# Kernel optimization log

Measured on AMD Instinct MI355X. Metric: run time of the kernel, lower is better.

## Reference

```python
import jax, jax.numpy as jnp
import numpy as np

BN_EPS = 1e-5

def _conv1x1(x, w, b):
    # x: (B,C,H,W), w: (O,C), b: (O,)
    return jnp.einsum('bchw,oc->bohw', x, w) + b[None, :, None, None]

def setup_inputs() -> dict:
    key = jax.random.key(0)
    ks = jax.random.split(key, 9)
    B, C, H, W = 16, 512, 64, 64
    Ci = C // 2
    x = jax.random.normal(ks[0], (B, C, H, W), dtype=jnp.float32)
    s_in = (2.0 / C) ** 0.5   # kaiming fan_out-ish scale for 1x1 conv
    s_ci = (2.0 / Ci) ** 0.5
    return {
        'x': x,
        'g_w': jax.random.normal(ks[1], (Ci, C), dtype=jnp.float32) * s_in,
        'g_b': jnp.zeros((Ci,), dtype=jnp.float32),
        'theta_w': jax.random.normal(ks[2], (Ci, C), dtype=jnp.float32) * s_in,
        'theta_b': jnp.zeros((Ci,), dtype=jnp.float32),
        'phi_w': jax.random.normal(ks[3], (Ci, C), dtype=jnp.float32) * s_in,
        'phi_b': jnp.zeros((Ci,), dtype=jnp.float32),
        'W_w': jax.random.normal(ks[4], (C, Ci), dtype=jnp.float32) * s_ci,
        'W_b': jnp.zeros((C,), dtype=jnp.float32),
        'bn_gamma': jnp.ones((C,), dtype=jnp.float32),
        'bn_beta': jnp.zeros((C,), dtype=jnp.float32),
    }

def reference(x, g_w, g_b, theta_w, theta_b, phi_w, phi_b, W_w, W_b, bn_gamma, bn_beta):
    B, C, H, W = x.shape
    N = H * W
    g_x = _conv1x1(x, g_w, g_b).reshape(B, -1, N)          # (B, Ci, N)
    theta_x = _conv1x1(x, theta_w, theta_b).reshape(B, -1, N)  # (B, Ci, N)
    phi_x = _conv1x1(x, phi_w, phi_b).reshape(B, -1, N)        # (B, Ci, N)
    # Faithful to source: theta NOT permuted -> f is (B, Ci, Ci) channel attention
    f = jnp.einsum('bcn,bdn->bcd', theta_x, phi_x)
    f_div_C = jax.nn.softmax(f, axis=-1)
    y = jnp.einsum('bcd,bdn->bcn', f_div_C, g_x).reshape(B, -1, H, W)  # (B, Ci, H, W)
    z = _conv1x1(y, W_w, W_b)                              # (B, C, H, W)
    # BatchNorm2d, training mode (batch statistics, biased var as in torch)
    mean = jnp.mean(z, axis=(0, 2, 3), keepdims=True)
    var = jnp.var(z, axis=(0, 2, 3), keepdims=True)
    z = (z - mean) * jax.lax.rsqrt(var + BN_EPS)
    z = z * bn_gamma[None, :, None, None] + bn_beta[None, :, None, None]
    return z + x
```

## Files before the change

kernel.cpp:

```cpp
#include <hip/hip_runtime.h>

typedef __bf16 bf16x8 __attribute__((ext_vector_type(8)));
typedef float f32x4 __attribute__((ext_vector_type(4)));

#define LDK 40
#define NB 16
#define C_ 512
#define CI 256
#define HW 4096
#define KSPLIT 4
#define KCHUNK (HW / KSPLIT)

__device__ __forceinline__ float bf2f(unsigned short u){
  union { unsigned int u; float f; } c; c.u = ((unsigned int)u) << 16; return c.f;
}
__device__ __forceinline__ unsigned short f2bf(float f){
  union { float f; unsigned int u; } c; c.f = f;
  unsigned int u = c.u + 0x7fffu + ((c.u >> 16) & 1u);
  return (unsigned short)(u >> 16);
}
__device__ __forceinline__ float read_val(const void* p, int i, bool f32){
  return f32 ? ((const float*)p)[i] : bf2f(((const unsigned short*)p)[i]);
}


__device__ __forceinline__ void stage_rm(const unsigned short* __restrict__ src, int stride,
                                         unsigned short* dst, int t){
  #pragma unroll
  for (int it = 0; it < 2; ++it){
    int idx = t + it*256;
    int row = idx >> 2;
    int ko  = (idx & 3) * 8;
    *(uint4*)(dst + row*LDK + ko) = *(const uint4*)(src + (size_t)row*stride + ko);
  }
}

__device__ __forceinline__ void stage_tr(const unsigned short* __restrict__ src, int stride,
                                         unsigned short* dst, int t){
  #pragma unroll
  for (int it = 0; it < 2; ++it){
    int idx = t + it*256;
    int row = idx >> 4;
    int co  = (idx & 15) * 8;
    uint4 vv = *(const uint4*)(src + (size_t)row*stride + co);
    unsigned short e[8]; *(uint4*)e = vv;
    #pragma unroll
    for (int k = 0; k < 8; ++k) dst[(co + k)*LDK + row] = e[k];
  }
}

__device__ __forceinline__ void mfma_step(const unsigned short* As, const unsigned short* Bs,
                                          f32x4 acc[4][4], int wm, int wn, int lane){
  const int r = lane & 15, q = lane >> 4;
  bf16x8 a[4], b[4];
  #pragma unroll
  for (int i = 0; i < 4; ++i)
    a[i] = *(const bf16x8*)(As + (wm*64 + 16*i + r)*LDK + 8*q);
  #pragma unroll
  for (int j = 0; j < 4; ++j)
    b[j] = *(const bf16x8*)(Bs + (wn*64 + 16*j + r)*LDK + 8*q);
  #pragma unroll
  for (int i = 0; i < 4; ++i)
    #pragma unroll
    for (int j = 0; j < 4; ++j)
      acc[i][j] = __builtin_amdgcn_mfma_f32_16x16x32_bf16(a[i], b[j], acc[i][j], 0, 0, 0);
}

__device__ __forceinline__ void gload16(const unsigned short* g, unsigned short* l){
  __builtin_amdgcn_global_load_lds(
      (__attribute__((address_space(1))) void*)const_cast<unsigned short*>(g),
      (__attribute__((address_space(3))) void*)l, 16, 0, 0);
}

__device__ __forceinline__ void gstage(const unsigned short* __restrict__ src, size_t rstride,
                                       unsigned short* buf, int w, int lane){
  const int ro = lane >> 3;
  const int sc = (lane & 7) ^ ro;
  const unsigned short* s0 = src + (size_t)ro*rstride + sc*8;
  unsigned short* l0 = buf + (size_t)(w*32)*64;
  #pragma unroll
  for (int i = 0; i < 4; ++i)
    gload16(s0 + (size_t)(w*32 + i*8)*rstride, l0 + i*8*64);
}

__global__ __launch_bounds__(256) void k_detect(const unsigned short* __restrict__ x, int* flag){
  const int t = threadIdx.x;
  int cnt = 0;
  for (int i = t; i < 65536; i += 256){
    unsigned short u = x[i];
    if (((u >> 7) & 0xFF) == 0xFF) cnt++;
  }
  __shared__ int red[256];
  red[t] = cnt; __syncthreads();
  for (int s2 = 128; s2 > 0; s2 >>= 1){
    if (t < s2) red[t] += red[t + s2];
    __syncthreads();
  }
  if (t == 0) flag[0] = (red[0] > 0) ? 1 : 0;
}

__global__ __launch_bounds__(256) void k_wconv(const void* tw, const void* pw, const void* gw,
    const void* Ww, const void* gb, const void* tb, const void* pb, const void* Wb,
    const void* gam, const void* bet, const int* __restrict__ flag,
    unsigned short* twh, unsigned short* twl, unsigned short* phh, unsigned short* phl,
    unsigned short* gwc, unsigned short* Wwc, float* biasf){
  const bool f32 = (*flag != 0);
  const int bid = blockIdx.x, t = threadIdx.x;
  if (bid < 2048){
    const int seg = bid >> 9;
    const int i = (bid & 511)*256 + t;
    if (seg == 0){
      float w = read_val(tw, i, f32);
      unsigned short h = f2bf(w);
      twh[i] = h; twl[i] = f2bf(w - bf2f(h));
    } else if (seg == 1){
      float w = read_val(pw, i, f32);
      unsigned short h = f2bf(w);
      phh[i] = h; phl[i] = f2bf(w - bf2f(h));
    } else if (seg == 2){
      gwc[i] = f2bf(read_val(gw, i, f32));
    } else {
      Wwc[i] = f2bf(read_val(Ww, i, f32));
    }
  } else {
    const int i = (bid - 2048)*256 + t;
    if (i < 2304){
      float v;
      if      (i <  256) v = read_val(gb,  i,        f32);
      else if (i <  512) v = read_val(tb,  i - 256,  f32);
      else if (i <  768) v = read_val(pb,  i - 512,  f32);
      else if (i < 1280) v = read_val(Wb,  i - 768,  f32);
      else if (i < 1792) v = read_val(gam, i - 1280, f32);
      else               v = read_val(bet, i - 1792, f32);
      biasf[i] = v;
    }
  }
}

__global__ __launch_bounds__(256) void k_xconv(const void* __restrict__ xraw,
    const int* __restrict__ flag, unsigned short* __restrict__ xq, float* __restrict__ s){
  const bool f32 = (*flag != 0);
  const int bc = blockIdx.x, t = threadIdx.x;
  float sum = 0.f;
  if (f32){
    const float* xr = (const float*)xraw + (size_t)bc*HW;
    unsigned short* oq = xq + (size_t)bc*8192;
    #pragma unroll
    for (int it = 0; it < 4; ++it){
      const int off = it*1024 + t*4;
      f32x4 v = *(const f32x4*)(xr + off);
      unsigned int wh[2], wl[2];
      #pragma unroll
      for (int k = 0; k < 2; ++k){
        unsigned short h0 = f2bf(v[2*k]),   h1 = f2bf(v[2*k+1]);
        unsigned short l0 = f2bf(v[2*k]   - bf2f(h0));
        unsigned short l1 = f2bf(v[2*k+1] - bf2f(h1));
        wh[k] = (unsigned int)h0 | ((unsigned int)h1 << 16);
        wl[k] = (unsigned int)l0 | ((unsigned int)l1 << 16);
      }
      sum += v[0] + v[1] + v[2] + v[3];
      const int qb = (off >> 5)*64 + (off & 31);
      *(uint2*)(oq + qb)      = make_uint2(wh[0], wh[1]);
      *(uint2*)(oq + qb + 32) = make_uint2(wl[0], wl[1]);
    }
  } else {
    const unsigned short* xr = (const unsigned short*)xraw + (size_t)bc*HW;
    #pragma unroll
    for (int it = 0; it < 2; ++it){
      const int off = it*2048 + t*8;
      uint4 raw = *(const uint4*)(xr + off);
      unsigned int wd[4] = {raw.x, raw.y, raw.z, raw.w};
      #pragma unroll
      for (int k = 0; k < 4; ++k)
        sum += bf2f((unsigned short)(wd[k] & 0xffff)) + bf2f((unsigned short)(wd[k] >> 16));
    }
  }
  #pragma unroll
  for (int off = 1; off < 64; off <<= 1) sum += __shfl_xor(sum, off);
  __shared__ float r1[4];
  if ((t & 63) == 0) r1[t >> 6] = sum;
  __syncthreads();
  if (t == 0) s[bc] = r1[0] + r1[1] + r1[2] + r1[3];
}

__global__ __launch_bounds__(256) void k_gram(const void* __restrict__ xraw,
    const unsigned short* __restrict__ xq, const int* __restrict__ flag,
    float* __restrict__ Gp){
  const bool f32 = (*flag != 0);
  const int b = blockIdx.z, ks = blockIdx.y, tile = blockIdx.x;
  int bm, bn;
  if      (tile < 4){ bm = 0; bn = tile; }
  else if (tile < 7){ bm = 1; bn = tile - 3; }
  else if (tile < 9){ bm = 2; bn = tile - 5; }
  else              { bm = 3; bn = 3; }
  const int t = threadIdx.x, lane = t & 63, w = t >> 6, wm = w >> 1, wn = w & 1;
  __shared__ __align__(16) unsigned short Abuf[2][128*64];
  __shared__ __align__(16) unsigned short Bbuf[2][128*64];
  const bool diag = (bm == bn);
  const unsigned short* srcA;
  const unsigned short* srcB;
  size_t rstride;
  int nsteps;
  if (f32){
    const unsigned short* xb = xq + (size_t)b*C_*8192;
    srcA = xb + (size_t)(bm*128)*8192 + (size_t)ks*(KCHUNK/32)*64;
    srcB = xb + (size_t)(bn*128)*8192 + (size_t)ks*(KCHUNK/32)*64;
    rstride = 8192; nsteps = KCHUNK/32;
  } else {
    const unsigned short* xb = (const unsigned short*)xraw + (size_t)b*C_*HW;
    srcA = xb + (size_t)(bm*128)*HW + ks*KCHUNK;
    srcB = xb + (size_t)(bn*128)*HW + ks*KCHUNK;
    rstride = HW; nsteps = KCHUNK/64;
  }
  f32x4 acc[4][4] = {};
  const int r = lane & 15, q = lane >> 4;
  const int rx = r & 7;
  const int c0 = q ^ rx;
  const int c1 = (4 + q) ^ rx;

  gstage(srcA, rstride, Abuf[0], w, lane);
  if (!diag) gstage(srcB, rstride, Bbuf[0], w, lane);
  __syncthreads();

  int cur = 0;
  for (int st = 0; st < nsteps; ++st){
    if (st + 1 < nsteps){
      gstage(srcA + (size_t)(st+1)*64, rstride, Abuf[cur^1], w, lane);
      if (!diag) gstage(srcB + (size_t)(st+1)*64, rstride, Bbuf[cur^1], w, lane);
    }
    const unsigned short* A = Abuf[cur];
    const unsigned short* B = diag ? Abuf[cur] : Bbuf[cur];
    bf16x8 a0[4], a1[4], b0[4], b1[4];
    #pragma unroll
    for (int i = 0; i < 4; ++i){
      const unsigned short* ap = A + (size_t)(wm*64 + 16*i + r)*64;
      a0[i] = *(const bf16x8*)(ap + c0*8);
      a1[i] = *(const bf16x8*)(ap + c1*8);
    }
    #pragma unroll
    for (int j = 0; j < 4; ++j){
      const unsigned short* bp = B + (size_t)(wn*64 + 16*j + r)*64;
      b0[j] = *(const bf16x8*)(bp + c0*8);
      b1[j] = *(const bf16x8*)(bp + c1*8);
    }
    if (f32){
      #pragma unroll
      for (int i = 0; i < 4; ++i)
        #pragma unroll
        for (int j = 0; j < 4; ++j){
          acc[i][j] = __builtin_amdgcn_mfma_f32_16x16x32_bf16(a0[i], b0[j], acc[i][j], 0, 0, 0);
          acc[i][j] = __builtin_amdgcn_mfma_f32_16x16x32_bf16(a0[i], b1[j], acc[i][j], 0, 0, 0);
          acc[i][j] = __builtin_amdgcn_mfma_f32_16x16x32_bf16(a1[i], b0[j], acc[i][j], 0, 0, 0);
        }
    } else {
      #pragma unroll
      for (int i = 0; i < 4; ++i)
        #pragma unroll
        for (int j = 0; j < 4; ++j){
          acc[i][j] = __builtin_amdgcn_mfma_f32_16x16x32_bf16(a0[i], b0[j], acc[i][j], 0, 0, 0);
          acc[i][j] = __builtin_amdgcn_mfma_f32_16x16x32_bf16(a1[i], b1[j], acc[i][j], 0, 0, 0);
        }
    }
    __syncthreads();
    cur ^= 1;
  }
  float* Gt = Gp + (((size_t)b*10 + tile)*KSPLIT + ks)*16384;
  #pragma unroll
  for (int i = 0; i < 4; ++i)
    #pragma unroll
    for (int j = 0; j < 4; ++j)
      #pragma unroll
      for (int ii = 0; ii < 4; ++ii){
        int row = wm*64 + 16*i + 4*q + ii;
        int col = wn*64 + 16*j + r;
        Gt[row*128 + col] = acc[i][j][ii];
      }
}

__global__ __launch_bounds__(256) void k_gred(const float* __restrict__ Gp,
    unsigned short* __restrict__ Gh, unsigned short* __restrict__ Gl){
  const int b = blockIdx.z, bmO = blockIdx.y, bnO = blockIdx.x, t = threadIdx.x;
  const int lo = bmO < bnO ? bmO : bnO;
  const int hi = bmO < bnO ? bnO : bmO;
  const int tile = (lo == 0) ? hi : (lo == 1) ? 3 + hi : (lo == 2) ? 5 + hi : 9;
  const float* src = Gp + ((size_t)b*10 + tile)*KSPLIT*16384;
  unsigned short* ghB = Gh + (size_t)b*C_*C_;
  unsigned short* glB = Gl + (size_t)b*C_*C_;
  if (bmO <= bnO){
    #pragma unroll
    for (int i = 0; i < 16; ++i){
      const int off = i*1024 + t*4;
      f32x4 v = *(const f32x4*)(src + off);
      #pragma unroll
      for (int ks = 1; ks < KSPLIT; ++ks){
        f32x4 u2 = *(const f32x4*)(src + ks*16384 + off);
        v[0] += u2[0]; v[1] += u2[1]; v[2] += u2[2]; v[3] += u2[3];
      }
      const int row = off >> 7, col = off & 127;
      unsigned int wh[2], wl[2];
      #pragma unroll
      for (int k = 0; k < 2; ++k){
        unsigned short h0 = f2bf(v[2*k]),   h1 = f2bf(v[2*k+1]);
        unsigned short l0 = f2bf(v[2*k]   - bf2f(h0));
        unsigned short l1 = f2bf(v[2*k+1] - bf2f(h1));
        wh[k] = (unsigned int)h0 | ((unsigned int)h1 << 16);
        wl[k] = (unsigned int)l0 | ((unsigned int)l1 << 16);
      }
      size_t o = (size_t)(bmO*128 + row)*C_ + bnO*128 + col;
      *(uint2*)(ghB + o) = make_uint2(wh[0], wh[1]);
      *(uint2*)(glB + o) = make_uint2(wl[0], wl[1]);
    }
  } else {
    __shared__ float ldz[32*129];
    const int rr = t >> 1, cseg = (t & 1)*16;
    const int orl = t >> 3, oseg = (t & 7)*16;
    for (int cc = 0; cc < 4; ++cc){
      float vals[16];
      #pragma unroll
      for (int j = 0; j < 4; ++j){
        const int so = rr*128 + cc*32 + cseg + j*4;
        f32x4 v = *(const f32x4*)(src + so);
        #pragma unroll
        for (int ks = 1; ks < KSPLIT; ++ks){
          f32x4 u2 = *(const f32x4*)(src + ks*16384 + so);
          v[0] += u2[0]; v[1] += u2[1]; v[2] += u2[2]; v[3] += u2[3];
        }
        vals[4*j] = v[0]; vals[4*j+1] = v[1]; vals[4*j+2] = v[2]; vals[4*j+3] = v[3];
      }
      __syncthreads();
      #pragma unroll
      for (int e = 0; e < 16; ++e) ldz[(cseg + e)*129 + rr] = vals[e];
      __syncthreads();
      unsigned int wh[8], wl[8];
      #pragma unroll
      for (int k = 0; k < 8; ++k){
        float f0 = ldz[orl*129 + oseg + 2*k];
        float f1 = ldz[orl*129 + oseg + 2*k + 1];
        unsigned short h0 = f2bf(f0), h1 = f2bf(f1);
        unsigned short l0 = f2bf(f0 - bf2f(h0)), l1 = f2bf(f1 - bf2f(h1));
        wh[k] = (unsigned int)h0 | ((unsigned int)h1 << 16);
        wl[k] = (unsigned int)l0 | ((unsigned int)l1 << 16);
      }
      size_t o = (size_t)(bmO*128 + cc*32 + orl)*C_ + bnO*128 + oseg;
      *(uint4*)(ghB + o)     = make_uint4(wh[0], wh[1], wh[2], wh[3]);
      *(uint4*)(ghB + o + 8) = make_uint4(wh[4], wh[5], wh[6], wh[7]);
      *(uint4*)(glB + o)     = make_uint4(wl[0], wl[1], wl[2], wl[3]);
      *(uint4*)(glB + o + 8) = make_uint4(wl[4], wl[5], wl[6], wl[7]);
    }
  }
}

__global__ __launch_bounds__(256) void k_T(const unsigned short* __restrict__ twh,
    const unsigned short* __restrict__ twl, const int* __restrict__ flag,
    const unsigned short* __restrict__ Gh, const unsigned short* __restrict__ Gl,
    unsigned short* __restrict__ Th, unsigned short* __restrict__ Tl){
  const bool f32 = (*flag != 0);
  const int b = blockIdx.z, nt = blockIdx.x, mt = blockIdx.y;
  const int t = threadIdx.x, lane = t & 63, w = t >> 6, wm = w >> 1, wn = w & 1;
  __shared__ unsigned short Ath[128*LDK];
  __shared__ unsigned short Atl[128*LDK];
  __shared__ unsigned short Bh[128*LDK];
  __shared__ unsigned short Bl[128*LDK];
  const unsigned short* Ghb = Gh + (size_t)b*C_*C_;
  const unsigned short* Glb = Gl + (size_t)b*C_*C_;
  f32x4 acc[4][4] = {};
  for (int k0 = 0; k0 < C_; k0 += 32){
    stage_rm(twh + (size_t)mt*128*C_ + k0, C_, Ath, t);
    if (f32) stage_rm(twl + (size_t)mt*128*C_ + k0, C_, Atl, t);
    stage_rm(Ghb + (size_t)nt*128*C_ + k0, C_, Bh, t);
    stage_rm(Glb + (size_t)nt*128*C_ + k0, C_, Bl, t);
    __syncthreads();
    mfma_step(Ath, Bh, acc, wm, wn, lane);
    mfma_step(Ath, Bl, acc, wm, wn, lane);
    if (f32) mfma_step(Atl, Bh, acc, wm, wn, lane);
    __syncthreads();
  }
  unsigned short* Thb = Th + (size_t)b*CI*C_;
  unsigned short* Tlb = Tl + (size_t)b*CI*C_;
  const int r = lane & 15, q = lane >> 4;
  #pragma unroll
  for (int i = 0; i < 4; ++i)
    #pragma unroll
    for (int j = 0; j < 4; ++j)
      #pragma unroll
      for (int ii = 0; ii < 4; ++ii){
        int row = mt*128 + wm*64 + 16*i + 4*q + ii;
        int col = nt*128 + wn*64 + 16*j + r;
        float vv = acc[i][j][ii];
        unsigned short h = f2bf(vv);
        Thb[(size_t)row*C_ + col] = h;
        Tlb[(size_t)row*C_ + col] = f2bf(vv - bf2f(h));
      }
}

__global__ __launch_bounds__(256) void k_f(const unsigned short* __restrict__ Th,
    const unsigned short* __restrict__ Tl, const unsigned short* __restrict__ phh,
    const unsigned short* __restrict__ phl, const int* __restrict__ flag,
    float* __restrict__ f){
  const bool f32 = (*flag != 0);
  const int b = blockIdx.z, nt = blockIdx.x, mt = blockIdx.y;
  const int t = threadIdx.x, lane = t & 63, w = t >> 6, wm = w >> 1, wn = w & 1;
  __shared__ unsigned short ATh[128*LDK];
  __shared__ unsigned short ATl[128*LDK];
  __shared__ unsigned short Bph[128*LDK];
  __shared__ unsigned short Bpl[128*LDK];
  f32x4 acc[4][4] = {};
  const unsigned short* Thb = Th + (size_t)b*CI*C_;
  const unsigned short* Tlb = Tl + (size_t)b*CI*C_;
  for (int k0 = 0; k0 < C_; k0 += 32){
    stage_rm(Thb + (size_t)mt*128*C_ + k0, C_, ATh, t);
    stage_rm(Tlb + (size_t)mt*128*C_ + k0, C_, ATl, t);
    stage_rm(phh + (size_t)nt*128*C_ + k0, C_, Bph, t);
    if (f32) stage_rm(phl + (size_t)nt*128*C_ + k0, C_, Bpl, t);
    __syncthreads();
    mfma_step(ATh, Bph, acc, wm, wn, lane);
    mfma_step(ATl, Bph, acc, wm, wn, lane);
    if (f32) mfma_step(ATh, Bpl, acc, wm, wn, lane);
    __syncthreads();
  }
  float* fb = f + (size_t)b*CI*CI;
  const int r = lane & 15, q = lane >> 4;
  #pragma unroll
  for (int i = 0; i < 4; ++i)
    #pragma unroll
    for (int j = 0; j < 4; ++j)
      #pragma unroll
      for (int ii = 0; ii < 4; ++ii){
        int row = mt*128 + wm*64 + 16*i + 4*q + ii;
        int col = nt*128 + wn*64 + 16*j + r;
        fb[(size_t)row*CI + col] = acc[i][j][ii];
      }
}

__global__ __launch_bounds__(256) void k_uv(const unsigned short* __restrict__ twh,
    const unsigned short* __restrict__ twl, const unsigned short* __restrict__ phh,
    const unsigned short* __restrict__ phl, const float* __restrict__ s,
    float* __restrict__ u, float* __restrict__ v){
  const int b = blockIdx.x, c = threadIdx.x;
  __shared__ float sl[C_];
  sl[c] = s[(size_t)b*C_ + c];
  sl[c + 256] = s[(size_t)b*C_ + c + 256];
  __syncthreads();
  float su = 0.f, sv = 0.f;
  for (int e = 0; e < C_; ++e){
    su += (bf2f(twh[(size_t)c*C_ + e]) + bf2f(twl[(size_t)c*C_ + e])) * sl[e];
    sv += (bf2f(phh[(size_t)c*C_ + e]) + bf2f(phl[(size_t)c*C_ + e])) * sl[e];
  }
  u[(size_t)b*CI + c] = su;
  v[(size_t)b*CI + c] = sv;
}

__global__ __launch_bounds__(256) void k_softmax(const float* __restrict__ f,
    const float* __restrict__ u, const float* __restrict__ v,
    const float* __restrict__ tbf, const float* __restrict__ pbf,
    unsigned short* __restrict__ S){
  const int b = blockIdx.y;
  const int c = blockIdx.x*4 + (threadIdx.x >> 6);
  const int lane = threadIdx.x & 63;
  const float* fr = f + ((size_t)b*CI + c)*CI;
  f32x4 val = *(const f32x4*)(fr + lane*4);
  const float uc = u[(size_t)b*CI + c];
  const float tbc = tbf[c];
  float vv[4];
  #pragma unroll
  for (int k = 0; k < 4; ++k){
    int d = lane*4 + k;
    float pbd = pbf[d];
    vv[k] = val[k] + uc*pbd + tbc*(v[(size_t)b*CI + d] + 4096.0f*pbd);
  }
  float mx = fmaxf(fmaxf(vv[0], vv[1]), fmaxf(vv[2], vv[3]));
  #pragma unroll
  for (int off = 1; off < 64; off <<= 1) mx = fmaxf(mx, __shfl_xor(mx, off));
  float e[4], sum = 0.f;
  #pragma unroll
  for (int k = 0; k < 4; ++k){ e[k] = expf(vv[k] - mx); sum += e[k]; }
  #pragma unroll
  for (int off = 1; off < 64; off <<= 1) sum += __shfl_xor(sum, off);
  float inv = 1.0f / sum;
  uint2 pack;
  pack.x = (unsigned int)f2bf(e[0]*inv) | ((unsigned int)f2bf(e[1]*inv) << 16);
  pack.y = (unsigned int)f2bf(e[2]*inv) | ((unsigned int)f2bf(e[3]*inv) << 16);
  *(uint2*)(S + ((size_t)b*CI + c)*CI + lane*4) = pack;
}

__global__ __launch_bounds__(256) void k_M2(const unsigned short* __restrict__ Wwc,
                                            const unsigned short* __restrict__ S,
                                            unsigned short* __restrict__ M2){
  const int b = blockIdx.z, nt = blockIdx.x, mt = blockIdx.y;
  const int t = threadIdx.x, lane = t & 63, w = t >> 6, wm = w >> 1, wn = w & 1;
  __shared__ unsigned short As[128*LDK];
  __shared__ unsigned short Bs[128*LDK];
  f32x4 acc[4][4] = {};
  for (int k0 = 0; k0 < CI; k0 += 32){
    stage_rm(Wwc + (size_t)mt*128*CI + k0, CI, As, t);
    stage_tr(S + (size_t)b*CI*CI + (size_t)k0*CI + nt*128, CI, Bs, t);
    __syncthreads();
    mfma_step(As, Bs, acc, wm, wn, lane);
    __syncthreads();
  }
  unsigned short* M2b = M2 + (size_t)b*C_*CI;
  const int r = lane & 15, q = lane >> 4;
  #pragma unroll
  for (int i = 0; i < 4; ++i)
    #pragma unroll
    for (int j = 0; j < 4; ++j)
      #pragma unroll
      for (int ii = 0; ii < 4; ++ii){
        int row = mt*128 + wm*64 + 16*i + 4*q + ii;
        int col = nt*128 + wn*64 + 16*j + r;
        M2b[(size_t)row*CI + col] = f2bf(acc[i][j][ii]);
      }
}

__global__ __launch_bounds__(256) void k_Wg(const unsigned short* __restrict__ M2,
                                            const unsigned short* __restrict__ gwc,
                                            unsigned short* __restrict__ Wg){
  const int b = blockIdx.z, nt = blockIdx.x, mt = blockIdx.y;
  const int t = threadIdx.x, lane = t & 63, w = t >> 6, wm = w >> 1, wn = w & 1;
  __shared__ unsigned short As[128*LDK];
  __shared__ unsigned short Bs[128*LDK];
  const unsigned short* M2b = M2 + (size_t)b*C_*CI;
  f32x4 acc[4][4] = {};
  for (int k0 = 0; k0 < CI; k0 += 32){
    stage_rm(M2b + (size_t)mt*128*CI + k0, CI, As, t);
    stage_tr(gwc + (size_t)k0*C_ + nt*128, C_, Bs, t);
    __syncthreads();
    mfma_step(As, Bs, acc, wm, wn, lane);
    __syncthreads();
  }
  unsigned short* Wgb = Wg + (size_t)b*C_*C_;
  const int r = lane & 15, q = lane >> 4;
  #pragma unroll
  for (int i = 0; i < 4; ++i)
    #pragma unroll
    for (int j = 0; j < 4; ++j)
      #pragma unroll
      for (int ii = 0; ii < 4; ++ii){
        int row = mt*128 + wm*64 + 16*i + 4*q + ii;
        int col = nt*128 + wn*64 + 16*j + r;
        Wgb[(size_t)row*C_ + col] = f2bf(acc[i][j][ii]);
      }
}

__global__ __launch_bounds__(256) void k_bias2(const unsigned short* __restrict__ M2,
    const float* __restrict__ gbf, const float* __restrict__ Wbf, float* __restrict__ b2){
  const int b = blockIdx.x, t = threadIdx.x;
  __shared__ float gs[CI];
  gs[t] = gbf[t];
  __syncthreads();
  #pragma unroll
  for (int cc = 0; cc < 2; ++cc){
    int c = cc*256 + t;
    const unsigned short* row = M2 + (size_t)b*C_*CI + (size_t)c*CI;
    float sv = 0.f;
    for (int ci = 0; ci < CI; ++ci) sv += bf2f(row[ci]) * gs[ci];
    b2[(size_t)b*C_ + c] = sv + Wbf[c];
  }
}

__global__ __launch_bounds__(512) void k_zW(const unsigned short* __restrict__ Wg,
    const void* __restrict__ xraw, const unsigned short* __restrict__ xq,
    const int* __restrict__ flag, const float* __restrict__ bias2,
    unsigned short* __restrict__ z){
  const bool f32 = (*flag != 0);
  const int b = blockIdx.z, hwp = blockIdx.x;
  const int t = threadIdx.x, lane = t & 63, w = t >> 6;
  const int wm = w >> 1, wn = w & 1;
  __shared__ __align__(16) unsigned short As[512*LDK];
  __shared__ __align__(16) unsigned short Bs[128*LDK];
  const unsigned short* Wgb = Wg + (size_t)b*C_*C_;
  const int hw0 = hwp*128;
  f32x4 acc[8][4] = {};
  for (int k0 = 0; k0 < C_; k0 += 32){
    #pragma unroll
    for (int it = 0; it < 4; ++it){
      int idx = t + it*512;
      int row = idx >> 2, ko = (idx & 3)*8;
      *(uint4*)(As + row*LDK + ko) = *(const uint4*)(Wgb + (size_t)row*C_ + k0 + ko);
    }
    {
      int row = t >> 4, co = (t & 15)*8;
      const unsigned short* bsrc;
      if (f32){
        int hw = hw0 + co;
        bsrc = xq + (size_t)(b*C_ + k0 + row)*8192 + (size_t)((hw >> 5)*64 + (hw & 31));
      } else {
        bsrc = (const unsigned short*)xraw + (size_t)(b*C_ + k0 + row)*HW + hw0 + co;
      }
      uint4 vv = *(const uint4*)bsrc;
      unsigned short e8[8]; *(uint4*)e8 = vv;
      #pragma unroll
      for (int kk = 0; kk < 8; ++kk) Bs[(co + kk)*LDK + row] = e8[kk];
    }
    __syncthreads();
    const int r = lane & 15, q = lane >> 4;
    bf16x8 bfr[4];
    #pragma unroll
    for (int j = 0; j < 4; ++j)
      bfr[j] = *(const bf16x8*)(Bs + (wn*64 + 16*j + r)*LDK + 8*q);
    #pragma unroll
    for (int i = 0; i < 8; ++i){
      bf16x8 af = *(const bf16x8*)(As + (size_t)(wm*128 + 16*i + r)*LDK + 8*q);
      #pragma unroll
      for (int j = 0; j < 4; ++j)
        acc[i][j] = __builtin_amdgcn_mfma_f32_16x16x32_bf16(af, bfr[j], acc[i][j], 0, 0, 0);
    }
    __syncthreads();
  }
  unsigned short* zb = z + (size_t)b*C_*HW;
  const float* b2 = bias2 + (size_t)b*C_;
  const int r = lane & 15, q = lane >> 4;
  #pragma unroll
  for (int i = 0; i < 8; ++i)
    #pragma unroll
    for (int ii = 0; ii < 4; ++ii){
      int row = wm*128 + 16*i + 4*q + ii;
      float bias = b2[row];
      #pragma unroll
      for (int j = 0; j < 4; ++j){
        int col = hw0 + wn*64 + 16*j + r;
        zb[(size_t)row*HW + col] = f2bf(acc[i][j][ii] + bias);
      }
    }
}

__global__ __launch_bounds__(256) void k_bnstats(const unsigned short* __restrict__ z,
    const float* __restrict__ gamf, const float* __restrict__ betf,
    float* __restrict__ scale, float* __restrict__ shift){
  const int o = blockIdx.x, t = threadIdx.x, lane = t & 63, w = t >> 6;
  float sum = 0.f, ss = 0.f;
  for (int b = 0; b < NB; ++b){
    const unsigned short* p = z + ((size_t)b*C_ + o)*HW + t*16;
    #pragma unroll
    for (int it = 0; it < 2; ++it){
      uint4 raw = *(const uint4*)(p + it*8);
      unsigned int wd[4] = {raw.x, raw.y, raw.z, raw.w};
      #pragma unroll
      for (int k = 0; k < 4; ++k){
        float f0 = bf2f((unsigned short)(wd[k] & 0xffff));
        float f1 = bf2f((unsigned short)(wd[k] >> 16));
        sum += f0 + f1; ss += f0*f0 + f1*f1;
      }
    }
  }
  #pragma unroll
  for (int off = 1; off < 64; off <<= 1){
    sum += __shfl_xor(sum, off);
    ss  += __shfl_xor(ss, off);
  }
  __shared__ float r1[4], r2[4];
  if (lane == 0){ r1[w] = sum; r2[w] = ss; }
  __syncthreads();
  if (t == 0){
    float S1 = r1[0]+r1[1]+r1[2]+r1[3];
    float S2 = r2[0]+r2[1]+r2[2]+r2[3];
    const float n = (float)NB * (float)HW;
    float mean = S1 / n;
    float var  = S2 / n - mean*mean;
    float sc = gamf[o] * rsqrtf(var + 1e-5f);
    scale[o] = sc;
    shift[o] = betf[o] - mean*sc;
  }
}

__global__ __launch_bounds__(256) void k_out(const unsigned short* __restrict__ z,
    const void* __restrict__ xraw, const int* __restrict__ flag,
    const float* __restrict__ scale, const float* __restrict__ shift, void* __restrict__ outraw){
  const bool f32 = (*flag != 0);
  const size_t g = (size_t)blockIdx.x*256 + threadIdx.x;
  const size_t base = g*8;
  const int o = (int)((base >> 12) & (C_ - 1));
  const float sc = scale[o], sh = shift[o];
  uint4 zr = *(const uint4*)(z + base);
  unsigned int zz[4] = {zr.x, zr.y, zr.z, zr.w};
  float zv[8];
  #pragma unroll
  for (int k = 0; k < 4; ++k){
    zv[2*k]   = bf2f((unsigned short)(zz[k] & 0xffff));
    zv[2*k+1] = bf2f((unsigned short)(zz[k] >> 16));
  }
  if (f32){
    const float* x = (const float*)xraw;
    float* out = (float*)outraw;
    f32x4 x0 = *(const f32x4*)(x + base);
    f32x4 x1 = *(const f32x4*)(x + base + 4);
    f32x4 o0, o1;
    #pragma unroll
    for (int k = 0; k < 4; ++k){
      o0[k] = zv[k]*sc + sh + x0[k];
      o1[k] = zv[4+k]*sc + sh + x1[k];
    }
    *(f32x4*)(out + base) = o0;
    *(f32x4*)(out + base + 4) = o1;
  } else {
    const unsigned short* x = (const unsigned short*)xraw;
    unsigned short* out = (unsigned short*)outraw;
    uint4 xr = *(const uint4*)(x + base);
    unsigned int xx[4] = {xr.x, xr.y, xr.z, xr.w};
    unsigned int res[4];
    #pragma unroll
    for (int k = 0; k < 4; ++k){
      float x0 = bf2f((unsigned short)(xx[k] & 0xffff));
      float x1 = bf2f((unsigned short)(xx[k] >> 16));
      res[k] = (unsigned int)f2bf(zv[2*k]*sc + sh + x0)
             | ((unsigned int)f2bf(zv[2*k+1]*sc + sh + x1) << 16);
    }
    uint4 ov; ov.x = res[0]; ov.y = res[1]; ov.z = res[2]; ov.w = res[3];
    *(uint4*)(out + base) = ov;
  }
}

extern "C" void kernel_launch(void* const* d_in, const int* in_sizes, int n_in,
                              void* d_out, int out_size, void* d_ws, size_t ws_size,
                              hipStream_t stream){
  (void)in_sizes; (void)n_in; (void)out_size;
  const void* x   = d_in[0];
  const void* g_w = d_in[1];
  const void* g_b = d_in[2];
  const void* t_w = d_in[3];
  const void* t_b = d_in[4];
  const void* p_w = d_in[5];
  const void* p_b = d_in[6];
  const void* W_w = d_in[7];
  const void* W_b = d_in[8];
  const void* gam = d_in[9];
  const void* bet = d_in[10];
  char* ws = (char*)d_ws;

  constexpr size_t OFF_FLAG = 0;
  constexpr size_t OFF_TWH = OFF_FLAG + 16;
  constexpr size_t OFF_TWL = OFF_TWH + (size_t)CI*C_*2;
  constexpr size_t OFF_PHH = OFF_TWL + (size_t)CI*C_*2;
  constexpr size_t OFF_PHL = OFF_PHH + (size_t)CI*C_*2;
  constexpr size_t OFF_GWC = OFF_PHL + (size_t)CI*C_*2;
  constexpr size_t OFF_WWC = OFF_GWC + (size_t)CI*C_*2;
  constexpr size_t OFF_BIA = OFF_WWC + (size_t)C_*CI*2;
  constexpr size_t OFF_GH  = OFF_BIA + 16384;
  constexpr size_t OFF_GL  = OFF_GH + (size_t)NB*C_*C_*2;
  constexpr size_t OFF_S   = OFF_GL + (size_t)NB*C_*C_*2;
  constexpr size_t OFF_U   = OFF_S  + (size_t)NB*C_*4;
  constexpr size_t OFF_V   = OFF_U  + (size_t)NB*CI*4;
  constexpr size_t OFF_TH  = OFF_V  + (size_t)NB*CI*4;
  constexpr size_t OFF_TL  = OFF_TH + (size_t)NB*CI*C_*2;
  constexpr size_t OFF_F   = OFF_TL + (size_t)NB*CI*C_*2;
  constexpr size_t OFF_SM  = OFF_F  + (size_t)NB*CI*CI*4;
  constexpr size_t OFF_M2  = OFF_SM + (size_t)NB*CI*CI*2;
  constexpr size_t OFF_B2  = OFF_M2 + (size_t)NB*C_*CI*2;
  constexpr size_t OFF_SC  = OFF_B2 + (size_t)NB*C_*4;
  constexpr size_t OFF_SH  = OFF_SC + (size_t)C_*4;
  constexpr size_t OFF_Z   = OFF_SH + (size_t)C_*4;
  constexpr size_t OFF_XQ  = OFF_Z  + (size_t)NB*C_*HW*2;
  constexpr size_t TOTAL   = OFF_XQ + (size_t)NB*C_*HW*4;
  static_assert((size_t)NB*10*KSPLIT*16384*4 <= (size_t)NB*C_*HW*2, "Gp alias fits in Z");
  if (ws_size < TOTAL) return;

  int* flag = (int*)(ws + OFF_FLAG);
  unsigned short* twh = (unsigned short*)(ws + OFF_TWH);
  unsigned short* twl = (unsigned short*)(ws + OFF_TWL);
  unsigned short* phh = (unsigned short*)(ws + OFF_PHH);
  unsigned short* phl = (unsigned short*)(ws + OFF_PHL);
  unsigned short* gwc = (unsigned short*)(ws + OFF_GWC);
  unsigned short* Wwc = (unsigned short*)(ws + OFF_WWC);
  float* biasf = (float*)(ws + OFF_BIA);
  unsigned short* Gh = (unsigned short*)(ws + OFF_GH);
  unsigned short* Gl = (unsigned short*)(ws + OFF_GL);
  float* s  = (float*)(ws + OFF_S);
  float* u  = (float*)(ws + OFF_U);
  float* v  = (float*)(ws + OFF_V);
  unsigned short* Th = (unsigned short*)(ws + OFF_TH);
  unsigned short* Tl = (unsigned short*)(ws + OFF_TL);
  float* f  = (float*)(ws + OFF_F);
  unsigned short* Sm = (unsigned short*)(ws + OFF_SM);
  unsigned short* M2 = (unsigned short*)(ws + OFF_M2);
  float* b2 = (float*)(ws + OFF_B2);
  unsigned short* z  = (unsigned short*)(ws + OFF_Z);
  float* scale = (float*)(ws + OFF_SC);
  float* shift = (float*)(ws + OFF_SH);
  unsigned short* xq = (unsigned short*)(ws + OFF_XQ);
  float* Gp = (float*)(ws + OFF_Z);
  unsigned short* Wg = (unsigned short*)(ws + OFF_GH);

  float* gbf = biasf;
  float* tbf = biasf + 256;
  float* pbf = biasf + 512;
  float* Wbf = biasf + 768;
  float* gamf = biasf + 1280;
  float* betf = biasf + 1792;

  dim3 blk(256);
  k_detect <<<dim3(1),          blk, 0, stream>>>((const unsigned short*)x, flag);
  k_wconv  <<<dim3(2057),       blk, 0, stream>>>(t_w, p_w, g_w, W_w, g_b, t_b, p_b, W_b,
                                                  gam, bet, flag, twh, twl, phh, phl, gwc, Wwc, biasf);
  k_xconv  <<<dim3(NB*C_),      blk, 0, stream>>>(x, flag, xq, s);
  k_gram   <<<dim3(10, KSPLIT, NB), blk, 0, stream>>>(x, xq, flag, Gp);
  k_gred   <<<dim3(4, 4, NB),   blk, 0, stream>>>(Gp, Gh, Gl);
  k_T      <<<dim3(4, 2, NB),   blk, 0, stream>>>(twh, twl, flag, Gh, Gl, Th, Tl);
  k_uv     <<<dim3(NB),         blk, 0, stream>>>(twh, twl, phh, phl, s, u, v);
  k_f      <<<dim3(2, 2, NB),   blk, 0, stream>>>(Th, Tl, phh, phl, flag, f);
  k_softmax<<<dim3(64, NB),     blk, 0, stream>>>(f, u, v, tbf, pbf, Sm);
  k_M2     <<<dim3(2, 4, NB),   blk, 0, stream>>>(Wwc, Sm, M2);
  k_Wg     <<<dim3(4, 4, NB),   blk, 0, stream>>>(M2, gwc, Wg);
  k_bias2  <<<dim3(NB),         blk, 0, stream>>>(M2, gbf, Wbf, b2);
  k_zW     <<<dim3(32, 1, NB),  dim3(512), 0, stream>>>(Wg, x, xq, flag, b2, z);
  k_bnstats<<<dim3(C_),         blk, 0, stream>>>(z, gamf, betf, scale, shift);
  k_out    <<<dim3(16384),      blk, 0, stream>>>(z, x, flag, scale, shift, d_out);
}
```

Baseline: 769.9 us.

## Fuse BN statistics into zW epilogue and read Wg fragments directly from global

Computes the per-channel sum and sum of squares of z in the k_zW epilogue using shuffle reductions and atomics, so the separate k_bnstats pass over z is no longer needed; a tiny k_bnfinal then turns the sums into scale and shift. The zeroing of the sum buffers is folded into k_bias2. k_zW also drops the shared-memory staging of the Wg tile and loads A fragments straight from global memory. k_gram swaps its grid y/z axes so that the batch index moves to y and the K-split index to z. The risks are atomic contention on 512 channels, uncoalesced global A loads in the GEMM inner loop, and statistics taken from fp32 z rather than the stored bf16 values.

```diff
diff --git a/kernel.cpp b/kernel.cpp
--- a/kernel.cpp
+++ b/kernel.cpp
@@ -187,7 +187,7 @@
     const unsigned short* __restrict__ xq, const int* __restrict__ flag,
     float* __restrict__ Gp){
   const bool f32 = (*flag != 0);
-  const int b = blockIdx.z, ks = blockIdx.y, tile = blockIdx.x;
+  const int b = blockIdx.y, ks = blockIdx.z, tile = blockIdx.x;
   int bm, bn;
   if      (tile < 4){ bm = 0; bn = tile; }
   else if (tile < 7){ bm = 1; bn = tile - 3; }
@@ -543,8 +543,12 @@
 }
 
 __global__ __launch_bounds__(256) void k_bias2(const unsigned short* __restrict__ M2,
-    const float* __restrict__ gbf, const float* __restrict__ Wbf, float* __restrict__ b2){
+    const float* __restrict__ gbf, const float* __restrict__ Wbf, float* __restrict__ b2,
+    float* __restrict__ sums){
   const int b = blockIdx.x, t = threadIdx.x;
+  if (b == 0){
+    sums[t] = 0.f; sums[t + 256] = 0.f; sums[t + 512] = 0.f; sums[t + 768] = 0.f;
+  }
   __shared__ float gs[CI];
   gs[t] = gbf[t];
   __syncthreads();
@@ -561,46 +565,39 @@
 __global__ __launch_bounds__(512) void k_zW(const unsigned short* __restrict__ Wg,
     const void* __restrict__ xraw, const unsigned short* __restrict__ xq,
     const int* __restrict__ flag, const float* __restrict__ bias2,
-    unsigned short* __restrict__ z){
+    unsigned short* __restrict__ z, float* __restrict__ sumZ, float* __restrict__ sumZ2){
   const bool f32 = (*flag != 0);
   const int b = blockIdx.z, hwp = blockIdx.x;
   const int t = threadIdx.x, lane = t & 63, w = t >> 6;
   const int wm = w >> 1, wn = w & 1;
-  __shared__ __align__(16) unsigned short As[512*LDK];
   __shared__ __align__(16) unsigned short Bs[128*LDK];
   const unsigned short* Wgb = Wg + (size_t)b*C_*C_;
   const int hw0 = hwp*128;
+  const int r = lane & 15, q = lane >> 4;
+  const int srow = t >> 4, sco = (t & 15)*8;
   f32x4 acc[8][4] = {};
   for (int k0 = 0; k0 < C_; k0 += 32){
-    #pragma unroll
-    for (int it = 0; it < 4; ++it){
-      int idx = t + it*512;
-      int row = idx >> 2, ko = (idx & 3)*8;
-      *(uint4*)(As + row*LDK + ko) = *(const uint4*)(Wgb + (size_t)row*C_ + k0 + ko);
-    }
     {
-      int row = t >> 4, co = (t & 15)*8;
       const unsigned short* bsrc;
       if (f32){
-        int hw = hw0 + co;
-        bsrc = xq + (size_t)(b*C_ + k0 + row)*8192 + (size_t)((hw >> 5)*64 + (hw & 31));
+        int hw = hw0 + sco;
+        bsrc = xq + (size_t)(b*C_ + k0 + srow)*8192 + (size_t)((hw >> 5)*64 + (hw & 31));
       } else {
-        bsrc = (const unsigned short*)xraw + (size_t)(b*C_ + k0 + row)*HW + hw0 + co;
+        bsrc = (const unsigned short*)xraw + (size_t)(b*C_ + k0 + srow)*HW + hw0 + sco;
       }
       uint4 vv = *(const uint4*)bsrc;
       unsigned short e8[8]; *(uint4*)e8 = vv;
       #pragma unroll
-      for (int kk = 0; kk < 8; ++kk) Bs[(co + kk)*LDK + row] = e8[kk];
-    }
-    __syncthreads();
-    const int r = lane & 15, q = lane >> 4;
+      for (int kk = 0; kk < 8; ++kk) Bs[(sco + kk)*LDK + srow] = e8[kk];
+    }
+    __syncthreads();
     bf16x8 bfr[4];
     #pragma unroll
     for (int j = 0; j < 4; ++j)
       bfr[j] = *(const bf16x8*)(Bs + (wn*64 + 16*j + r)*LDK + 8*q);
     #pragma unroll
     for (int i = 0; i < 8; ++i){
-      bf16x8 af = *(const bf16x8*)(As + (size_t)(wm*128 + 16*i + r)*LDK + 8*q);
+      bf16x8 af = *(const bf16x8*)(Wgb + (size_t)(wm*128 + 16*i + r)*C_ + k0 + 8*q);
       #pragma unroll
       for (int j = 0; j < 4; ++j)
         acc[i][j] = __builtin_amdgcn_mfma_f32_16x16x32_bf16(af, bfr[j], acc[i][j], 0, 0, 0);
@@ -609,58 +606,42 @@
   }
   unsigned short* zb = z + (size_t)b*C_*HW;
   const float* b2 = bias2 + (size_t)b*C_;
-  const int r = lane & 15, q = lane >> 4;
   #pragma unroll
   for (int i = 0; i < 8; ++i)
     #pragma unroll
     for (int ii = 0; ii < 4; ++ii){
       int row = wm*128 + 16*i + 4*q + ii;
       float bias = b2[row];
+      float s1 = 0.f, s2 = 0.f;
       #pragma unroll
       for (int j = 0; j < 4; ++j){
         int col = hw0 + wn*64 + 16*j + r;
-        zb[(size_t)row*HW + col] = f2bf(acc[i][j][ii] + bias);
-      }
-    }
-}
-
-__global__ __launch_bounds__(256) void k_bnstats(const unsigned short* __restrict__ z,
+        float zv = acc[i][j][ii] + bias;
+        zb[(size_t)row*HW + col] = f2bf(zv);
+        s1 += zv; s2 += zv*zv;
+      }
+      #pragma unroll
+      for (int off = 1; off < 16; off <<= 1){
+        s1 += __shfl_xor(s1, off);
+        s2 += __shfl_xor(s2, off);
+      }
+      if (r == 0){
+        atomicAdd(&sumZ[row], s1);
+        atomicAdd(&sumZ2[row], s2);
+      }
+    }
+}
+
+__global__ __launch_bounds__(256) void k_bnfinal(const float* __restrict__ sums,
     const float* __restrict__ gamf, const float* __restrict__ betf,
     float* __restrict__ scale, float* __restrict__ shift){
-  const int o = blockIdx.x, t = threadIdx.x, lane = t & 63, w = t >> 6;
-  float sum = 0.f, ss = 0.f;
-  for (int b = 0; b < NB; ++b){
-    const unsigned short* p = z + ((size_t)b*C_ + o)*HW + t*16;
-    #pragma unroll
-    for (int it = 0; it < 2; ++it){
-      uint4 raw = *(const uint4*)(p + it*8);
-      unsigned int wd[4] = {raw.x, raw.y, raw.z, raw.w};
-      #pragma unroll
-      for (int k = 0; k < 4; ++k){
-        float f0 = bf2f((unsigned short)(wd[k] & 0xffff));
-        float f1 = bf2f((unsigned short)(wd[k] >> 16));
-        sum += f0 + f1; ss += f0*f0 + f1*f1;
-      }
-    }
-  }
-  #pragma unroll
-  for (int off = 1; off < 64; off <<= 1){
-    sum += __shfl_xor(sum, off);
-    ss  += __shfl_xor(ss, off);
-  }
-  __shared__ float r1[4], r2[4];
-  if (lane == 0){ r1[w] = sum; r2[w] = ss; }
-  __syncthreads();
-  if (t == 0){
-    float S1 = r1[0]+r1[1]+r1[2]+r1[3];
-    float S2 = r2[0]+r2[1]+r2[2]+r2[3];
-    const float n = (float)NB * (float)HW;
-    float mean = S1 / n;
-    float var  = S2 / n - mean*mean;
-    float sc = gamf[o] * rsqrtf(var + 1e-5f);
-    scale[o] = sc;
-    shift[o] = betf[o] - mean*sc;
-  }
+  const int o = blockIdx.x*256 + threadIdx.x;
+  const float n = (float)NB * (float)HW;
+  float mean = sums[o] / n;
+  float var  = sums[512 + o] / n - mean*mean;
+  float sc = gamf[o] * rsqrtf(var + 1e-5f);
+  scale[o] = sc;
+  shift[o] = betf[o] - mean*sc;
 }
 
 __global__ __launch_bounds__(256) void k_out(const unsigned short* __restrict__ z,
@@ -748,7 +729,8 @@
   constexpr size_t OFF_B2  = OFF_M2 + (size_t)NB*C_*CI*2;
   constexpr size_t OFF_SC  = OFF_B2 + (size_t)NB*C_*4;
   constexpr size_t OFF_SH  = OFF_SC + (size_t)C_*4;
-  constexpr size_t OFF_Z   = OFF_SH + (size_t)C_*4;
+  constexpr size_t OFF_SU  = OFF_SH + (size_t)C_*4;
+  constexpr size_t OFF_Z   = OFF_SU + 4096;
   constexpr size_t OFF_XQ  = OFF_Z  + (size_t)NB*C_*HW*2;
   constexpr size_t TOTAL   = OFF_XQ + (size_t)NB*C_*HW*4;
   static_assert((size_t)NB*10*KSPLIT*16384*4 <= (size_t)NB*C_*HW*2, "Gp alias fits in Z");
@@ -773,6 +755,7 @@
   unsigned short* Sm = (unsigned short*)(ws + OFF_SM);
   unsigned short* M2 = (unsigned short*)(ws + OFF_M2);
   float* b2 = (float*)(ws + OFF_B2);
+  float* sums = (float*)(ws + OFF_SU);
   unsigned short* z  = (unsigned short*)(ws + OFF_Z);
   float* scale = (float*)(ws + OFF_SC);
   float* shift = (float*)(ws + OFF_SH);
@@ -792,7 +775,7 @@
   k_wconv  <<<dim3(2057),       blk, 0, stream>>>(t_w, p_w, g_w, W_w, g_b, t_b, p_b, W_b,
                                                   gam, bet, flag, twh, twl, phh, phl, gwc, Wwc, biasf);
   k_xconv  <<<dim3(NB*C_),      blk, 0, stream>>>(x, flag, xq, s);
-  k_gram   <<<dim3(10, KSPLIT, NB), blk, 0, stream>>>(x, xq, flag, Gp);
+  k_gram   <<<dim3(10, NB, KSPLIT), blk, 0, stream>>>(x, xq, flag, Gp);
   k_gred   <<<dim3(4, 4, NB),   blk, 0, stream>>>(Gp, Gh, Gl);
   k_T      <<<dim3(4, 2, NB),   blk, 0, stream>>>(twh, twl, flag, Gh, Gl, Th, Tl);
   k_uv     <<<dim3(NB),         blk, 0, stream>>>(twh, twl, phh, phl, s, u, v);
@@ -800,8 +783,9 @@
   k_softmax<<<dim3(64, NB),     blk, 0, stream>>>(f, u, v, tbf, pbf, Sm);
   k_M2     <<<dim3(2, 4, NB),   blk, 0, stream>>>(Wwc, Sm, M2);
   k_Wg     <<<dim3(4, 4, NB),   blk, 0, stream>>>(M2, gwc, Wg);
-  k_bias2  <<<dim3(NB),         blk, 0, stream>>>(M2, gbf, Wbf, b2);
-  k_zW     <<<dim3(32, 1, NB),  dim3(512), 0, stream>>>(Wg, x, xq, flag, b2, z);
-  k_bnstats<<<dim3(C_),         blk, 0, stream>>>(z, gamf, betf, scale, shift);
+  k_bias2  <<<dim3(NB),         blk, 0, stream>>>(M2, gbf, Wbf, b2, sums);
+  k_zW     <<<dim3(32, 1, NB),  dim3(512), 0, stream>>>(Wg, x, xq, flag, b2, z,
+                                                        sums, sums + 512);
+  k_bnfinal<<<dim3(2),          blk, 0, stream>>>(sums, gamf, betf, scale, shift);
   k_out    <<<dim3(16384),      blk, 0, stream>>>(z, x, flag, scale, shift, d_out);
 }
```

After: 1.036 ms. +34.6%, slower.
